# Kernel optimization log

Hardware: AMD Instinct MI355X
Metric: run time of the kernel (lower is better)

The kernel has to match this reference:

```python
import jax, jax.numpy as jnp
import numpy as np

N, D = 32768, 512          # rows, input dim (row count 32-aligned per source)
C, K = 16, 16              # ncodebooks, codewords per codebook (4-bit codes)
S = D // C                 # subvector length per codebook
M = 1024                   # output columns (W_test.shape[1])


def setup_inputs() -> dict:
    key = jax.random.key(0)
    k1, k2, k3 = jax.random.split(key, 3)
    X = jax.random.normal(k1, (N, D), dtype=jnp.float32)
    protos = jax.random.normal(k2, (C, K, S), dtype=jnp.float32)
    luts = jax.random.normal(k3, (C, K, M), dtype=jnp.float32)
    return {"X": X, "protos": protos, "luts": luts}


def reference(X, protos, luts):
    n, d = X.shape
    c, k, s = protos.shape
    # --- PQ encode: nearest prototype per codebook subvector ---
    Xr = X.reshape(n, c, s)                                   # [N, C, S]
    dots = jnp.einsum("ncs,cks->nck", Xr, protos)             # [N, C, K]
    dists = (protos * protos).sum(-1)[None, :, :] - 2.0 * dots
    codes = jnp.argmin(dists, axis=-1)                        # [N, C] int codes
    # --- LUT gather-accumulate: out[n,m] = sum_c luts[c, codes[n,c], m] ---
    onehot = jax.nn.one_hot(codes, k, dtype=luts.dtype)       # [N, C, K]
    out = jnp.einsum("nck,ckm->nm", onehot, luts)             # [N, M]
    # forward() scales the approximate product by mean(X)
    return out * jnp.mean(X)
```

## Files before the change

### kernel.cpp

```cpp
#include <hip/hip_runtime.h>
#include <hip/hip_bf16.h>
#include <stdint.h>
#include <string.h>

#define N_ROWS 32768
#define DIM    512
#define CB     16
#define KW     16
#define SV     32
#define MCOLS  1024

#define LROW   264

typedef __attribute__((ext_vector_type(8))) short bf16x8_t;
typedef __attribute__((ext_vector_type(4))) float f32x4_t;


__global__ __launch_bounds__(256) void prep_kernel(
    const float* __restrict__ protos, double* __restrict__ protos_d,
    double* __restrict__ norms_d)
{
    const int tid = threadIdx.x;
    #pragma unroll
    for (int j = 0; j < 32; ++j) {
        const int idx = j * 256 + tid;
        protos_d[idx] = (double)protos[idx];
    }
    const float* src = protos + tid * SV;
    double nk = 0.0;
    #pragma unroll
    for (int j = 0; j < SV; ++j) { double v = (double)src[j]; nk += v * v; }
    norms_d[tid] = nk;
}

__global__ __launch_bounds__(256, 4) void encode_kernel(
    const float* __restrict__ X, const double* __restrict__ protos_d,
    const double* __restrict__ norms_d, uint8_t* __restrict__ codes,
    double* __restrict__ sum_out)
{
    __shared__ double redsum[4];

    const int tid  = threadIdx.x;
    const int lane = tid & 63;
    const int wv   = tid >> 6;
    const int c    = blockIdx.x & 15;
    const int row  = (blockIdx.x >> 4) * 256 + tid;

    const float* xp = X + (size_t)row * DIM + c * SV;
    double xd[SV];
    double sx = 0.0;
    #pragma unroll
    for (int j = 0; j < 8; ++j) {
        float4 v = *(const float4*)(xp + j * 4);
        xd[j * 4 + 0] = (double)v.x; xd[j * 4 + 1] = (double)v.y;
        xd[j * 4 + 2] = (double)v.z; xd[j * 4 + 3] = (double)v.w;
        sx += (double)v.x + (double)v.y + (double)v.z + (double)v.w;
    }

    const double* __restrict__ Pd = protos_d + (size_t)c * (KW * SV);
    const double* __restrict__ Nd = norms_d + (size_t)c * KW;

    double best = 1e300;
    int bk = 0;
    #pragma unroll
    for (int k = 0; k < KW; ++k) {
        const double* pk = Pd + k * SV;
        double d0 = 0.0, d1 = 0.0, d2 = 0.0, d3 = 0.0;
        #pragma unroll
        for (int s = 0; s < 8; ++s) {
            d0 += xd[4 * s + 0] * pk[4 * s + 0];
            d1 += xd[4 * s + 1] * pk[4 * s + 1];
            d2 += xd[4 * s + 2] * pk[4 * s + 2];
            d3 += xd[4 * s + 3] * pk[4 * s + 3];
        }
        double dist = Nd[k] - 2.0 * ((d0 + d1) + (d2 + d3));
        if (dist < best) { best = dist; bk = k; }
    }
    codes[(size_t)row * CB + c] = (uint8_t)bk;

    #pragma unroll
    for (int off = 32; off > 0; off >>= 1) sx += __shfl_down(sx, off);
    if (lane == 0) redsum[wv] = sx;
    __syncthreads();
    if (tid == 0) {
        double s = redsum[0] + redsum[1] + redsum[2] + redsum[3];
        atomicAdd(sum_out, s);
    }
}

__global__ __launch_bounds__(256, 4) void lut_mfma_kernel(
    const float* __restrict__ luts, const uint8_t* __restrict__ codes,
    const double* __restrict__ sum_in, float* __restrict__ out)
{
    __shared__ uint16_t lut_s[64 * LROW];
    __shared__ uint8_t  codes_s[512 * 16];
    __shared__ uint4    tbl[32];

    const int tid   = threadIdx.x;
    const int mtile = blockIdx.x & 15;
    const int nblk  = blockIdx.x >> 4;
    const int m0 = mtile * 64;
    const int n0 = nblk * 512;

    const float scale = (float)(sum_in[0] * (1.0 / ((double)N_ROWS * (double)DIM)));

    if (tid < 32) {
        const int sel = tid >> 4, code = tid & 15;
        const int t = code - sel * 8;
        uint32_t d[4] = {0u, 0u, 0u, 0u};
        if (t >= 0 && t < 8) d[t >> 1] = 0x3F80u << ((t & 1) * 16);
        tbl[tid] = make_uint4(d[0], d[1], d[2], d[3]);
    }

    {
        const uint4* src = (const uint4*)(codes + (size_t)n0 * CB);
        uint4* dst = (uint4*)codes_s;
        dst[tid]       = src[tid];
        dst[tid + 256] = src[tid + 256];
    }

    for (int i = tid; i < 256 * 64; i += 256) {
        const int ck = i >> 6, m = i & 63;
        float v = luts[(size_t)ck * MCOLS + m0 + m] * scale;
        __hip_bfloat16 b = __float2bfloat16(v);
        lut_s[m * LROW + ck] = *(const uint16_t*)&b;
    }
    __syncthreads();

    const int wv   = tid >> 6;
    const int lane = tid & 63;
    const int mloc = lane & 15;
    const int half = lane >> 4;
    const int sel  = half & 1;
    const int h2   = half >> 1;
    const int shiftbase = h2 * 8;

    #pragma unroll
    for (int rtq = 0; rtq < 2; ++rtq) {
        const int rowbase = wv * 128 + rtq * 64;

        uint4 crow[4];
        #pragma unroll
        for (int rt = 0; rt < 4; ++rt)
            crow[rt] = *(const uint4*)(codes_s + (rowbase + rt * 16 + mloc) * 16);

        f32x4_t acc[4][4];
        #pragma unroll
        for (int rt = 0; rt < 4; ++rt)
            #pragma unroll
            for (int ct = 0; ct < 4; ++ct)
                acc[rt][ct] = (f32x4_t){0.f, 0.f, 0.f, 0.f};

        #pragma unroll
        for (int ki = 0; ki < 8; ++ki) {
            bf16x8_t bf[4];
            #pragma unroll
            for (int ct = 0; ct < 4; ++ct) {
                const uint16_t* bp = lut_s + (ct * 16 + mloc) * LROW
                                   + ki * 32 + half * 8;
                bf[ct] = *reinterpret_cast<const bf16x8_t*>(bp);
            }
            #pragma unroll
            for (int rt = 0; rt < 4; ++rt) {
                const uint32_t cws[4] = {crow[rt].x, crow[rt].y,
                                         crow[rt].z, crow[rt].w};
                const uint32_t code =
                    (cws[ki >> 1] >> (shiftbase + (ki & 1) * 16)) & 0xffu;
                const bf16x8_t af =
                    *reinterpret_cast<const bf16x8_t*>(&tbl[sel * 16 + code]);
                #pragma unroll
                for (int ct = 0; ct < 4; ++ct)
                    acc[rt][ct] = __builtin_amdgcn_mfma_f32_16x16x32_bf16(
                        af, bf[ct], acc[rt][ct], 0, 0, 0);
            }
        }

        #pragma unroll
        for (int rt = 0; rt < 4; ++rt) {
            const int grow = n0 + rowbase + rt * 16 + half * 4;
            #pragma unroll
            for (int reg = 0; reg < 4; ++reg) {
                float* op = out + (size_t)(grow + reg) * MCOLS + m0 + mloc;
                #pragma unroll
                for (int ct = 0; ct < 4; ++ct)
                    op[ct * 16] = acc[rt][ct][reg];
            }
        }
    }
}

extern "C" void kernel_launch(void* const* d_in, const int* in_sizes, int n_in,
                              void* d_out, int out_size, void* d_ws, size_t ws_size,
                              hipStream_t stream) {
    const float* X      = (const float*)d_in[0];
    const float* protos = (const float*)d_in[1];
    const float* luts   = (const float*)d_in[2];
    float* out = (float*)d_out;

    double*  sum_ws   = (double*)d_ws;
    double*  protos_d = (double*)((uint8_t*)d_ws + 256);
    double*  norms_d  = (double*)((uint8_t*)d_ws + 66048);
    uint8_t* codes    = (uint8_t*)d_ws + 68352;

    hipMemsetAsync(d_ws, 0, 8, stream);

    prep_kernel<<<dim3(1), dim3(256), 0, stream>>>(protos, protos_d, norms_d);

    encode_kernel<<<dim3(2048), dim3(256), 0, stream>>>(X, protos_d, norms_d,
                                                        codes, sum_ws);

    lut_mfma_kernel<<<dim3(1024), dim3(256), 0, stream>>>(luts, codes, sum_ws, out);
}
```

Measured before the change: 225.3 us.

## Stage X through swizzled LDS, swizzle LUT tile, compute one-hot in registers

The encode kernel now loads each block's X slab cooperatively with coalesced float4 reads into an XOR-swizzled shared buffer, then each thread reads its own row from LDS. Before, each thread read a strided 128-byte chunk directly from global memory. The LUT kernel drops the padded LUT row stride in favour of an XOR swizzle to avoid bank conflicts. It also reads codes straight from global memory instead of staging them in LDS, and builds the one-hot A fragment with register arithmetic instead of a table lookup. This removes LDS traffic and a sync dependency, but adds ALU work per MFMA and uncached-style global code loads.

New measurement: 224.1 us. No clear change (-0.5%).

```diff
diff --git a/kernel.cpp b/kernel.cpp
--- a/kernel.cpp
+++ b/kernel.cpp
@@ -10,8 +10,6 @@
 #define SV     32
 #define MCOLS  1024
 
-#define LROW   264
-
 typedef __attribute__((ext_vector_type(8))) short bf16x8_t;
 typedef __attribute__((ext_vector_type(4))) float f32x4_t;
 
@@ -38,23 +36,36 @@
     const double* __restrict__ norms_d, uint8_t* __restrict__ codes,
     double* __restrict__ sum_out)
 {
+    __shared__ __align__(16) float xs[256 * 32];
     __shared__ double redsum[4];
 
     const int tid  = threadIdx.x;
     const int lane = tid & 63;
     const int wv   = tid >> 6;
     const int c    = blockIdx.x & 15;
-    const int row  = (blockIdx.x >> 4) * 256 + tid;
-
-    const float* xp = X + (size_t)row * DIM + c * SV;
+    const int n0   = (blockIdx.x >> 4) * 256;
+
+    double sx = 0.0;
+    {
+        const int ch = tid & 7;
+        const int rr = tid >> 3;
+        #pragma unroll
+        for (int it = 0; it < 8; ++it) {
+            const int row = it * 32 + rr;
+            const float4 v = *(const float4*)(X + (size_t)(n0 + row) * DIM
+                                              + c * SV + ch * 4);
+            *(float4*)&xs[row * 32 + ((ch ^ (row & 7)) << 2)] = v;
+            sx += (double)v.x + (double)v.y + (double)v.z + (double)v.w;
+        }
+    }
+    __syncthreads();
+
     double xd[SV];
-    double sx = 0.0;
     #pragma unroll
     for (int j = 0; j < 8; ++j) {
-        float4 v = *(const float4*)(xp + j * 4);
+        const float4 v = *(const float4*)&xs[tid * 32 + ((j ^ (tid & 7)) << 2)];
         xd[j * 4 + 0] = (double)v.x; xd[j * 4 + 1] = (double)v.y;
         xd[j * 4 + 2] = (double)v.z; xd[j * 4 + 3] = (double)v.w;
-        sx += (double)v.x + (double)v.y + (double)v.z + (double)v.w;
     }
 
     const double* __restrict__ Pd = protos_d + (size_t)c * (KW * SV);
@@ -76,7 +87,7 @@
         double dist = Nd[k] - 2.0 * ((d0 + d1) + (d2 + d3));
         if (dist < best) { best = dist; bk = k; }
     }
-    codes[(size_t)row * CB + c] = (uint8_t)bk;
+    codes[(size_t)(n0 + tid) * CB + c] = (uint8_t)bk;
 
     #pragma unroll
     for (int off = 32; off > 0; off >>= 1) sx += __shfl_down(sx, off);
@@ -92,9 +103,7 @@
     const float* __restrict__ luts, const uint8_t* __restrict__ codes,
     const double* __restrict__ sum_in, float* __restrict__ out)
 {
-    __shared__ uint16_t lut_s[64 * LROW];
-    __shared__ uint8_t  codes_s[512 * 16];
-    __shared__ uint4    tbl[32];
+    __shared__ __align__(16) uint16_t lut_s[64 * 256];
 
     const int tid   = threadIdx.x;
     const int mtile = blockIdx.x & 15;
@@ -104,26 +113,11 @@
 
     const float scale = (float)(sum_in[0] * (1.0 / ((double)N_ROWS * (double)DIM)));
 
-    if (tid < 32) {
-        const int sel = tid >> 4, code = tid & 15;
-        const int t = code - sel * 8;
-        uint32_t d[4] = {0u, 0u, 0u, 0u};
-        if (t >= 0 && t < 8) d[t >> 1] = 0x3F80u << ((t & 1) * 16);
-        tbl[tid] = make_uint4(d[0], d[1], d[2], d[3]);
-    }
-
-    {
-        const uint4* src = (const uint4*)(codes + (size_t)n0 * CB);
-        uint4* dst = (uint4*)codes_s;
-        dst[tid]       = src[tid];
-        dst[tid + 256] = src[tid + 256];
-    }
-
     for (int i = tid; i < 256 * 64; i += 256) {
         const int ck = i >> 6, m = i & 63;
         float v = luts[(size_t)ck * MCOLS + m0 + m] * scale;
         __hip_bfloat16 b = __float2bfloat16(v);
-        lut_s[m * LROW + ck] = *(const uint16_t*)&b;
+        lut_s[m * 256 + (ck ^ ((m & 7) << 3))] = *(const uint16_t*)&b;
     }
     __syncthreads();
 
@@ -134,6 +128,8 @@
     const int sel  = half & 1;
     const int h2   = half >> 1;
     const int shiftbase = h2 * 8;
+    const int sel8 = sel * 8;
+    const int swz  = (mloc & 7) << 3;
 
     #pragma unroll
     for (int rtq = 0; rtq < 2; ++rtq) {
@@ -142,7 +138,8 @@
         uint4 crow[4];
         #pragma unroll
         for (int rt = 0; rt < 4; ++rt)
-            crow[rt] = *(const uint4*)(codes_s + (rowbase + rt * 16 + mloc) * 16);
+            crow[rt] = *(const uint4*)(codes
+                         + (size_t)(n0 + rowbase + rt * 16 + mloc) * CB);
 
         f32x4_t acc[4][4];
         #pragma unroll
@@ -154,10 +151,10 @@
         #pragma unroll
         for (int ki = 0; ki < 8; ++ki) {
             bf16x8_t bf[4];
+            const int kidx = (ki * 32 + half * 8) ^ swz;
             #pragma unroll
             for (int ct = 0; ct < 4; ++ct) {
-                const uint16_t* bp = lut_s + (ct * 16 + mloc) * LROW
-                                   + ki * 32 + half * 8;
+                const uint16_t* bp = lut_s + (ct * 16 + mloc) * 256 + kidx;
                 bf[ct] = *reinterpret_cast<const bf16x8_t*>(bp);
             }
             #pragma unroll
@@ -166,12 +163,16 @@
                                          crow[rt].z, crow[rt].w};
                 const uint32_t code =
                     (cws[ki >> 1] >> (shiftbase + (ki & 1) * 16)) & 0xffu;
-                const bf16x8_t af =
-                    *reinterpret_cast<const bf16x8_t*>(&tbl[sel * 16 + code]);
+                const int t = (int)code - sel8;
+                const uint64_t sh = 0x3F80ull << ((t & 3) * 16);
+                const int q = t >> 2;
+                union { uint64_t u[2]; bf16x8_t v8; } A;
+                A.u[0] = (q == 0) ? sh : 0ull;
+                A.u[1] = (q == 1) ? sh : 0ull;
                 #pragma unroll
                 for (int ct = 0; ct < 4; ++ct)
                     acc[rt][ct] = __builtin_amdgcn_mfma_f32_16x16x32_bf16(
-                        af, bf[ct], acc[rt][ct], 0, 0, 0);
+                        A.v8, bf[ct], acc[rt][ct], 0, 0, 0);
             }
         }
 
```
